# Kernel optimization log

Measured on AMD Instinct MI355X. Metric: run time of the kernel, lower is better.

## Reference

```python
import jax, jax.numpy as jnp
import numpy as np

N_HEAD = 8
WINDOW = 22   # sliding window size from get_mask()
TRAIN = 29    # per-segment length cap from get_mask()


def _build_mask(T):
    # Banded (sliding-window causal) mask on one segment, tiled 3x3 over segments.
    t = T // 3
    m = np.triu(np.ones((TRAIN, TRAIN), dtype=bool), 1)
    for i in range(WINDOW, TRAIN):
        m[i, : i - WINDOW + 1] = True
    m = np.tile(m[:t, :t], (3, 3))  # [T, T], True = masked out
    return jnp.asarray(m)


def setup_inputs() -> dict:
    key = jax.random.key(0)
    ks = jax.random.split(key, 5)
    B, T, C = 512, 87, 512
    s = 0.02
    return {
        "x": jax.random.normal(ks[0], (B, T, C), dtype=jnp.float32),
        "Wq": jax.random.normal(ks[1], (C, C), dtype=jnp.float32) * s,
        "bq": jnp.zeros((C,), dtype=jnp.float32),
        "Wk": jax.random.normal(ks[2], (C, C), dtype=jnp.float32) * s,
        "bk": jnp.zeros((C,), dtype=jnp.float32),
        "Wv": jax.random.normal(ks[3], (C, C), dtype=jnp.float32) * s,
        "bv": jnp.zeros((C,), dtype=jnp.float32),
        "Wp": jax.random.normal(ks[4], (C, C), dtype=jnp.float32) * s,
        "bp": jnp.zeros((C,), dtype=jnp.float32),
    }


def reference(x, Wq, bq, Wk, bk, Wv, bv, Wp, bp):
    B, T, C = x.shape
    H = N_HEAD
    D = C // H
    # nn.Linear: y = x @ W.T + b
    def split_heads(y):
        return y.reshape(B, T, H, D).transpose(0, 2, 1, 3)  # [B,H,T,D]
    q = split_heads(x @ Wq.T + bq)
    k = split_heads(x @ Wk.T + bk)
    v = split_heads(x @ Wv.T + bv)
    att = jnp.einsum("bhqd,bhkd->bhqk", q, k) * (1.0 / jnp.sqrt(jnp.float32(D)))
    mask = _build_mask(T)  # [T,T] True = disallowed
    att = jnp.where(mask[None, None], -jnp.inf, att)
    att = jax.nn.softmax(att, axis=-1)
    # dropout layers are identity in eval mode
    y = jnp.einsum("bhqk,bhkd->bhqd", att, v)
    y = y.transpose(0, 2, 1, 3).reshape(B, T, C)
    return y @ Wp.T + bp
```

## Files before the change

kernel.cpp:

```cpp
#include <hip/hip_runtime.h>
#include <hip/hip_bf16.h>
#include <stdint.h>

#define B_   512
#define T_   87
#define C_   512
#define H_   8
#define D_   64
#define BT_  44544
#define BH_  4096

typedef __attribute__((ext_vector_type(4))) float f32x4;
typedef __attribute__((ext_vector_type(8))) __bf16 bf16x8;
typedef __attribute__((ext_vector_type(4))) unsigned short u16x4;

__device__ __forceinline__ int mod29(int x) {
  return x < 29 ? x : (x < 58 ? x - 29 : x - 58);
}


__global__ void convert_x_kernel(const float* __restrict__ x,
                                 __hip_bfloat16* __restrict__ xb, int n4) {
  int stride = gridDim.x * blockDim.x;
  for (int i = blockIdx.x * blockDim.x + threadIdx.x; i < n4; i += stride) {
    f32x4 v = ((const f32x4*)x)[i];
    u16x4 o;
    o.x = __builtin_bit_cast(unsigned short, __float2bfloat16(v.x));
    o.y = __builtin_bit_cast(unsigned short, __float2bfloat16(v.y));
    o.z = __builtin_bit_cast(unsigned short, __float2bfloat16(v.z));
    o.w = __builtin_bit_cast(unsigned short, __float2bfloat16(v.w));
    ((u16x4*)xb)[i] = o;
  }
}

__global__ void convert_w_kernel(const float* __restrict__ Wq, const float* __restrict__ Wk,
                                 const float* __restrict__ Wv, const float* __restrict__ Wp,
                                 const float* __restrict__ bq, const float* __restrict__ bk,
                                 const float* __restrict__ bv,
                                 __hip_bfloat16* __restrict__ wqkv,
                                 __hip_bfloat16* __restrict__ wp,
                                 float* __restrict__ biasc) {
  const int NW = 262144;
  const int total = 3 * NW + NW + 1536;
  int stride = gridDim.x * blockDim.x;
  for (int i = blockIdx.x * blockDim.x + threadIdx.x; i < total; i += stride) {
    if (i < 3 * NW) {
      float v = (i < NW) ? Wq[i] : (i < 2 * NW ? Wk[i - NW] : Wv[i - 2 * NW]);
      wqkv[i] = __float2bfloat16(v);
    } else if (i < 4 * NW) {
      wp[i - 3 * NW] = __float2bfloat16(Wp[i - 3 * NW]);
    } else {
      int j = i - 4 * NW;
      biasc[j] = (j < 512) ? bq[j] : (j < 1024 ? bk[j - 512] : bv[j - 1024]);
    }
  }
}


template<int EPI>
__global__ __launch_bounds__(256, 4) void gemms_kernel(
    const __hip_bfloat16* __restrict__ A, const __hip_bfloat16* __restrict__ Bt,
    const float* __restrict__ bias, int ntn,
    void* __restrict__ o0, void* __restrict__ o1, void* __restrict__ o2) {
  __shared__ __align__(16) char smem[2][2][8192];

  int tid = threadIdx.x, lane = tid & 63, wave = tid >> 6;
  int r16 = lane & 15, r4 = lane >> 4;

  int nwg = gridDim.x;
  int wg = (blockIdx.x & 7) * (nwg >> 3) + (blockIdx.x >> 3);
  int tileM = (wg / ntn) * 128, tileN = (wg % ntn) * 128;

  int wr = wave >> 1, wc = wave & 1;
  int wbM = wr * 64, wbN = wc * 64;

  const int rl = tid >> 2, c = tid & 3;
  const char* Ag = (const char*)A + (size_t)(tileM + rl) * 1024 + c * 16;
  const char* Bg = (const char*)Bt + (size_t)(tileN + rl) * 1024 + c * 16;
  int lsl[2];
#pragma unroll
  for (int j = 0; j < 2; ++j) {
    int row = rl + 64 * j;
    lsl[j] = row * 64 + ((c ^ ((row >> 1) & 3)) << 4);
  }

  int aoff[4], boff[4];
#pragma unroll
  for (int f = 0; f < 4; ++f) {
    int ra = wbM + f * 16 + r16;
    int rb = wbN + f * 16 + r16;
    aoff[f] = ra * 64 + ((r4 ^ ((ra >> 1) & 3)) << 4);
    boff[f] = rb * 64 + ((r4 ^ ((rb >> 1) & 3)) << 4);
  }

  f32x4 acc[4][4] = {};
  bf16x8 sA[2], sB[2];

#pragma unroll
  for (int j = 0; j < 2; ++j) {
    sA[j] = *(const bf16x8*)(Ag + (size_t)j * 65536);
    sB[j] = *(const bf16x8*)(Bg + (size_t)j * 65536);
  }
#pragma unroll
  for (int j = 0; j < 2; ++j) {
    *(bf16x8*)(&smem[0][0][0] + lsl[j]) = sA[j];
    *(bf16x8*)(&smem[0][1][0] + lsl[j]) = sB[j];
  }
  __syncthreads();

#pragma unroll
  for (int kt = 0; kt < 16; ++kt) {
    const int cur = kt & 1;
    if (kt < 15) {
#pragma unroll
      for (int j = 0; j < 2; ++j) {
        sA[j] = *(const bf16x8*)(Ag + (size_t)j * 65536 + (kt + 1) * 64);
        sB[j] = *(const bf16x8*)(Bg + (size_t)j * 65536 + (kt + 1) * 64);
      }
    }
    {
      const char* Ab = &smem[cur][0][0];
      const char* Bb = &smem[cur][1][0];
      bf16x8 bfr[4];
#pragma unroll
      for (int fn = 0; fn < 4; ++fn) bfr[fn] = *(const bf16x8*)(Bb + boff[fn]);
      __builtin_amdgcn_s_setprio(1);
#pragma unroll
      for (int fm = 0; fm < 4; ++fm) {
        bf16x8 a = *(const bf16x8*)(Ab + aoff[fm]);
#pragma unroll
        for (int fn = 0; fn < 4; ++fn)
          acc[fm][fn] = __builtin_amdgcn_mfma_f32_16x16x32_bf16(a, bfr[fn],
                                                                acc[fm][fn], 0, 0, 0);
      }
      __builtin_amdgcn_s_setprio(0);
    }
    if (kt < 15) {
#pragma unroll
      for (int j = 0; j < 2; ++j) {
        *(bf16x8*)(&smem[cur ^ 1][0][0] + lsl[j]) = sA[j];
        *(bf16x8*)(&smem[cur ^ 1][1][0] + lsl[j]) = sB[j];
      }
    }
    __syncthreads();
  }

  if constexpr (EPI == 0) {
    char* scratch = &smem[0][0][0] + wave * 2304;
    int gn0 = tileN + wbN;
    int sel = gn0 >> 9;
    int hh = (gn0 & 511) >> 6;
    __hip_bfloat16* obase = (sel == 0) ? (__hip_bfloat16*)o0
                          : (sel == 1) ? (__hip_bfloat16*)o1 : (__hip_bfloat16*)o2;
#pragma unroll
    for (int fm = 0; fm < 4; ++fm) {
#pragma unroll
      for (int fn = 0; fn < 4; ++fn) {
        float bv = bias[gn0 + fn * 16 + r16];
#pragma unroll
        for (int rr = 0; rr < 4; ++rr)
          *(__hip_bfloat16*)(scratch + (r4 * 4 + rr) * 144 + (fn * 16 + r16) * 2) =
              __float2bfloat16(acc[fm][fn][rr] + bv);
      }
#pragma unroll
      for (int p = 0; p < 2; ++p) {
        bf16x8 vrow = *(const bf16x8*)(scratch + (p * 8 + (lane >> 3)) * 144 + (lane & 7) * 16);
        int gm = tileM + wbM + fm * 16 + p * 8 + (lane >> 3);
        int bb = gm / 87, tt = gm - bb * 87;
        *(bf16x8*)(obase + ((size_t)(bb * 8 + hh) * 96 + tt) * 64 + (lane & 7) * 8) = vrow;
      }
    }
  } else {
    char* scratch = &smem[0][0][0] + wave * 4352;
#pragma unroll
    for (int fm = 0; fm < 4; ++fm) {
#pragma unroll
      for (int fn = 0; fn < 4; ++fn) {
        float bv = bias[tileN + wbN + fn * 16 + r16];
#pragma unroll
        for (int rr = 0; rr < 4; ++rr)
          *(float*)(scratch + (r4 * 4 + rr) * 272 + (fn * 16 + r16) * 4) =
              acc[fm][fn][rr] + bv;
      }
#pragma unroll
      for (int p = 0; p < 4; ++p) {
        f32x4 vr = *(const f32x4*)(scratch + (p * 4 + (lane >> 4)) * 272 + (lane & 15) * 16);
        int gm = tileM + wbM + fm * 16 + p * 4 + (lane >> 4);
        *(f32x4*)((float*)o0 + (size_t)gm * 512 + tileN + wbN + (lane & 15) * 4) = vr;
      }
    }
  }
}

#define QS_O  0
#define KS_O  13824
#define VT_O  27648
#define PB_O  40960

__global__ __launch_bounds__(256) void attn_kernel(
    const __hip_bfloat16* __restrict__ q_ws, const __hip_bfloat16* __restrict__ k_ws,
    const __hip_bfloat16* __restrict__ v_ws, __hip_bfloat16* __restrict__ y_ws) {
  __shared__ __align__(16) char smem[60928];

  int tid = threadIdx.x, lane = tid & 63, wave = tid >> 6;
  int bh = blockIdx.x, b = bh >> 3, h = bh & 7;
  int r16 = lane & 15, r4 = lane >> 4;

  {
    const bf16x8* gq = (const bf16x8*)(q_ws + (size_t)bh * 6144);
    const bf16x8* gk = (const bf16x8*)(k_ws + (size_t)bh * 6144);
    const bf16x8* gv = (const bf16x8*)(v_ws + (size_t)bh * 6144);
    for (int i = tid; i < 768; i += 256) {
      int row = i >> 3, ch = i & 7;
      *(bf16x8*)(smem + QS_O + row * 144 + ch * 16) = gq[i];
      *(bf16x8*)(smem + KS_O + row * 144 + ch * 16) = gk[i];
      bf16x8 v8 = gv[i];
      int tc = row >> 3, tb = (row & 7) << 1, xr = ch & 3;
#pragma unroll
      for (int e = 0; e < 8; ++e) {
        int d = ch * 8 + e;
        *(__bf16*)(smem + VT_O + d * 208 + ((tc ^ xr) << 4) + tb) = v8[e];
      }
    }
  }
  __syncthreads();

  int ljv[6]; bool cok[6];
#pragma unroll
  for (int j = 0; j < 6; ++j) {
    int col = j * 16 + r16;
    ljv[j] = mod29(col);
    cok[j] = col < 87;
  }

  for (int m = wave; m < 6; m += 4) {
    f32x4 s[6] = {};
#pragma unroll
    for (int kk = 0; kk < 2; ++kk) {
      bf16x8 aq = *(const bf16x8*)(smem + QS_O + (m * 16 + r16) * 144 + kk * 64 + r4 * 16);
#pragma unroll
      for (int j = 0; j < 6; ++j) {
        bf16x8 kb = *(const bf16x8*)(smem + KS_O + (j * 16 + r16) * 144 + kk * 64 + r4 * 16);
        s[j] = __builtin_amdgcn_mfma_f32_16x16x32_bf16(aq, kb, s[j], 0, 0, 0);
      }
    }
#pragma unroll
    for (int rr = 0; rr < 4; ++rr) {
      int row = m * 16 + r4 * 4 + rr;
      bool rok = row < 87;
      int lr = mod29(row);
      float mxv = -1e30f;
#pragma unroll
      for (int j = 0; j < 6; ++j) {
        bool al = rok && cok[j] && (ljv[j] <= lr) && (ljv[j] + 21 >= lr);
        float sv = al ? s[j][rr] * 0.125f : -1e30f;
        s[j][rr] = sv;
        mxv = fmaxf(mxv, sv);
      }
      mxv = fmaxf(mxv, __shfl_xor(mxv, 1));
      mxv = fmaxf(mxv, __shfl_xor(mxv, 2));
      mxv = fmaxf(mxv, __shfl_xor(mxv, 4));
      mxv = fmaxf(mxv, __shfl_xor(mxv, 8));
      float sm = 0.f;
#pragma unroll
      for (int j = 0; j < 6; ++j) {
        float e = __expf(s[j][rr] - mxv);
        s[j][rr] = e;
        sm += e;
      }
      sm += __shfl_xor(sm, 1);
      sm += __shfl_xor(sm, 2);
      sm += __shfl_xor(sm, 4);
      sm += __shfl_xor(sm, 8);
      float inv = rok ? 1.f / sm : 0.f;
#pragma unroll
      for (int j = 0; j < 6; ++j)
        *(__hip_bfloat16*)(smem + PB_O + row * 208 + (j * 16 + r16) * 2) =
            __float2bfloat16(s[j][rr] * inv);
    }
  }
  __syncthreads();

  for (int p = 0; p < 6; ++p) {
    int pair = wave + p * 4;
    int mt = pair >> 2, nt = pair & 3;
    int d = nt * 16 + r16;
    int dx = (d >> 3) & 3;
    f32x4 acc = {0.f, 0.f, 0.f, 0.f};
#pragma unroll
    for (int kk = 0; kk < 3; ++kk) {
      bf16x8 a  = *(const bf16x8*)(smem + PB_O + (mt * 16 + r16) * 208 + kk * 64 + r4 * 16);
      bf16x8 bb = *(const bf16x8*)(smem + VT_O + d * 208 + (((kk * 4 + r4) ^ dx) << 4));
      acc = __builtin_amdgcn_mfma_f32_16x16x32_bf16(a, bb, acc, 0, 0, 0);
    }
    int t0 = mt * 16 + r4 * 4;
#pragma unroll
    for (int r = 0; r < 4; ++r)
      *(__bf16*)(smem + QS_O + (t0 + r) * 136 + d * 2) =
          __builtin_bit_cast(__bf16, __builtin_bit_cast(unsigned short, __float2bfloat16(acc[r])));
  }
  __syncthreads();

  for (int i = tid; i < 768; i += 256) {
    int row = i >> 3, ch = i & 7;
    if (row < 87) {
      bf16x8 vrow = *(const bf16x8*)(smem + QS_O + row * 136 + ch * 16);
      *(bf16x8*)((char*)y_ws + ((size_t)b * 87 + row) * 1024 + h * 128 + ch * 16) = vrow;
    }
  }
}

extern "C" void kernel_launch(void* const* d_in, const int* in_sizes, int n_in,
                              void* d_out, int out_size, void* d_ws, size_t ws_size,
                              hipStream_t stream) {
  const float* x  = (const float*)d_in[0];
  const float* Wq = (const float*)d_in[1];
  const float* bq = (const float*)d_in[2];
  const float* Wk = (const float*)d_in[3];
  const float* bk = (const float*)d_in[4];
  const float* Wv = (const float*)d_in[5];
  const float* bv = (const float*)d_in[6];
  const float* Wp = (const float*)d_in[7];
  const float* bp = (const float*)d_in[8];
  float* out = (float*)d_out;

  char* ws = (char*)d_ws;
  size_t off = 0;
  __hip_bfloat16* xb    = (__hip_bfloat16*)(ws + off); off += (size_t)BT_ * 512 * 2;
  __hip_bfloat16* wqkv  = (__hip_bfloat16*)(ws + off); off += 1536 * 512 * 2;
  __hip_bfloat16* wp    = (__hip_bfloat16*)(ws + off); off += 512 * 512 * 2;
  float*          biasc = (float*)(ws + off);          off += 8192;
  __hip_bfloat16* q_ws  = (__hip_bfloat16*)(ws + off); off += (size_t)BH_ * 6144 * 2;
  __hip_bfloat16* k_ws  = (__hip_bfloat16*)(ws + off); off += (size_t)BH_ * 6144 * 2;
  __hip_bfloat16* v_ws  = (__hip_bfloat16*)(ws + off); off += (size_t)BH_ * 6144 * 2;
  __hip_bfloat16* yb = xb;

  if (ws_size < off) return;

  convert_x_kernel<<<2048, 256, 0, stream>>>(x, xb, BT_ * 512 / 4);
  convert_w_kernel<<<1024, 256, 0, stream>>>(Wq, Wk, Wv, Wp, bq, bk, bv, wqkv, wp, biasc);
  gemms_kernel<0><<<4176, 256, 0, stream>>>(xb, wqkv, biasc, 12, q_ws, k_ws, v_ws);
  attn_kernel<<<BH_, 256, 0, stream>>>(q_ws, k_ws, v_ws, yb);
  gemms_kernel<1><<<1392, 256, 0, stream>>>(yb, wp, bp, 4, out, nullptr, nullptr);
}
```

Before: 239.5 us.

## Load GEMM tiles directly into LDS with global_load_lds and explicit waits

Replaces the register-staged global-to-LDS copy in both GEMMs with the direct global_load_lds path. The XOR swizzle moves from the LDS write address to the global source address, and the loop uses explicit vmcnt waits plus raw s_barrier with scheduling barriers. This is meant to save the VGPRs and ds_write instructions spent on staging, and launch bounds rise from 4 to 5 waves per SIMD to use the freed registers. The risk is correctness of the swizzle-to-source mapping and the barrier ordering around the overwritten buffer.

```diff
diff --git a/kernel.cpp b/kernel.cpp
--- a/kernel.cpp
+++ b/kernel.cpp
@@ -13,6 +13,19 @@
 typedef __attribute__((ext_vector_type(4))) float f32x4;
 typedef __attribute__((ext_vector_type(8))) __bf16 bf16x8;
 typedef __attribute__((ext_vector_type(4))) unsigned short u16x4;
+
+__device__ __forceinline__ void gl_lds16(const void* g, void* l) {
+  __builtin_amdgcn_global_load_lds(
+      (const __attribute__((address_space(1))) unsigned int*)g,
+      (__attribute__((address_space(3))) unsigned int*)l, 16, 0, 0);
+}
+
+template<int N>
+__device__ __forceinline__ void waitv() {
+  asm volatile("s_waitcnt vmcnt(%0)" :: "i"(N) : "memory");
+}
+
+#define PHASE_SEP() __builtin_amdgcn_sched_barrier(0)
 
 __device__ __forceinline__ int mod29(int x) {
   return x < 29 ? x : (x < 58 ? x - 29 : x - 58);
@@ -58,7 +71,7 @@
 
 
 template<int EPI>
-__global__ __launch_bounds__(256, 4) void gemms_kernel(
+__global__ __launch_bounds__(256, 5) void gemmg_kernel(
     const __hip_bfloat16* __restrict__ A, const __hip_bfloat16* __restrict__ Bt,
     const float* __restrict__ bias, int ntn,
     void* __restrict__ o0, void* __restrict__ o1, void* __restrict__ o2) {
@@ -74,14 +87,15 @@
   int wr = wave >> 1, wc = wave & 1;
   int wbM = wr * 64, wbN = wc * 64;
 
-  const int rl = tid >> 2, c = tid & 3;
-  const char* Ag = (const char*)A + (size_t)(tileM + rl) * 1024 + c * 16;
-  const char* Bg = (const char*)Bt + (size_t)(tileN + rl) * 1024 + c * 16;
-  int lsl[2];
+  const int rl0 = tid >> 2, cc = tid & 3;
+  const char* Asrc[2];
+  const char* Bsrc[2];
 #pragma unroll
   for (int j = 0; j < 2; ++j) {
-    int row = rl + 64 * j;
-    lsl[j] = row * 64 + ((c ^ ((row >> 1) & 3)) << 4);
+    int row = rl0 + 64 * j;
+    int colsw = ((cc ^ ((row >> 1) & 3)) << 4);
+    Asrc[j] = (const char*)A + (size_t)(tileM + row) * 1024 + colsw;
+    Bsrc[j] = (const char*)Bt + (size_t)(tileN + row) * 1024 + colsw;
   }
 
   int aoff[4], boff[4];
@@ -94,30 +108,27 @@
   }
 
   f32x4 acc[4][4] = {};
-  bf16x8 sA[2], sB[2];
-
-#pragma unroll
-  for (int j = 0; j < 2; ++j) {
-    sA[j] = *(const bf16x8*)(Ag + (size_t)j * 65536);
-    sB[j] = *(const bf16x8*)(Bg + (size_t)j * 65536);
-  }
-#pragma unroll
-  for (int j = 0; j < 2; ++j) {
-    *(bf16x8*)(&smem[0][0][0] + lsl[j]) = sA[j];
-    *(bf16x8*)(&smem[0][1][0] + lsl[j]) = sB[j];
-  }
-  __syncthreads();
+
+#define STAGE(bufi, kb)                                                         \
+  do {                                                                          \
+    _Pragma("unroll")                                                           \
+    for (int j = 0; j < 2; ++j)                                                 \
+      gl_lds16(Asrc[j] + (kb), &smem[bufi][0][0] + j * 4096 + wave * 1024);     \
+    _Pragma("unroll")                                                           \
+    for (int j = 0; j < 2; ++j)                                                 \
+      gl_lds16(Bsrc[j] + (kb), &smem[bufi][1][0] + j * 4096 + wave * 1024);     \
+  } while (0)
+
+  STAGE(0, 0);
 
 #pragma unroll
   for (int kt = 0; kt < 16; ++kt) {
     const int cur = kt & 1;
-    if (kt < 15) {
-#pragma unroll
-      for (int j = 0; j < 2; ++j) {
-        sA[j] = *(const bf16x8*)(Ag + (size_t)j * 65536 + (kt + 1) * 64);
-        sB[j] = *(const bf16x8*)(Bg + (size_t)j * 65536 + (kt + 1) * 64);
-      }
-    }
+    if (kt < 15) STAGE(cur ^ 1, (kt + 1) * 64);
+    if (kt < 15) waitv<4>(); else waitv<0>();
+    PHASE_SEP();
+    __builtin_amdgcn_s_barrier();
+    PHASE_SEP();
     {
       const char* Ab = &smem[cur][0][0];
       const char* Bb = &smem[cur][1][0];
@@ -135,15 +146,11 @@
       }
       __builtin_amdgcn_s_setprio(0);
     }
-    if (kt < 15) {
-#pragma unroll
-      for (int j = 0; j < 2; ++j) {
-        *(bf16x8*)(&smem[cur ^ 1][0][0] + lsl[j]) = sA[j];
-        *(bf16x8*)(&smem[cur ^ 1][1][0] + lsl[j]) = sB[j];
-      }
-    }
-    __syncthreads();
-  }
+    PHASE_SEP();
+    __builtin_amdgcn_s_barrier();
+    PHASE_SEP();
+  }
+#undef STAGE
 
   if constexpr (EPI == 0) {
     char* scratch = &smem[0][0][0] + wave * 2304;
@@ -339,7 +346,7 @@
 
   convert_x_kernel<<<2048, 256, 0, stream>>>(x, xb, BT_ * 512 / 4);
   convert_w_kernel<<<1024, 256, 0, stream>>>(Wq, Wk, Wv, Wp, bq, bk, bv, wqkv, wp, biasc);
-  gemms_kernel<0><<<4176, 256, 0, stream>>>(xb, wqkv, biasc, 12, q_ws, k_ws, v_ws);
+  gemmg_kernel<0><<<4176, 256, 0, stream>>>(xb, wqkv, biasc, 12, q_ws, k_ws, v_ws);
   attn_kernel<<<BH_, 256, 0, stream>>>(q_ws, k_ws, v_ws, yb);
-  gemms_kernel<1><<<1392, 256, 0, stream>>>(yb, wp, bp, 4, out, nullptr, nullptr);
-}
+  gemmg_kernel<1><<<1392, 256, 0, stream>>>(yb, wp, bp, 4, out, nullptr, nullptr);
+}
```

Measured after the change: 258.8 us. 1.08x slower.

## Use two-wave 128x128 GEMM tiles with 64x128 per-wave subtiles

Applied to the files above, without the earlier changes.

Restructures both projection GEMMs to run 128-thread workgroups, where each of two waves computes a 64x128 output subtile instead of four waves computing 64x64. The aim is more MFMA work per LDS load of B fragments, since each wave reuses its A fragment across eight B fragments. Global-to-LDS loading and the epilogue staging are reworked to match. The cost is doubled accumulator registers per wave and fewer waves per workgroup, which may reduce latency hiding. Scratch in the epilogue grows and must still fit inside the shared buffer.

```diff
diff --git a/kernel.cpp b/kernel.cpp
--- a/kernel.cpp
+++ b/kernel.cpp
@@ -58,7 +58,7 @@
 
 
 template<int EPI>
-__global__ __launch_bounds__(256, 4) void gemms_kernel(
+__global__ __launch_bounds__(128, 2) void gemm2w_kernel(
     const __hip_bfloat16* __restrict__ A, const __hip_bfloat16* __restrict__ Bt,
     const float* __restrict__ bias, int ntn,
     void* __restrict__ o0, void* __restrict__ o1, void* __restrict__ o2) {
@@ -71,38 +71,42 @@
   int wg = (blockIdx.x & 7) * (nwg >> 3) + (blockIdx.x >> 3);
   int tileM = (wg / ntn) * 128, tileN = (wg % ntn) * 128;
 
-  int wr = wave >> 1, wc = wave & 1;
-  int wbM = wr * 64, wbN = wc * 64;
-
-  const int rl = tid >> 2, c = tid & 3;
-  const char* Ag = (const char*)A + (size_t)(tileM + rl) * 1024 + c * 16;
-  const char* Bg = (const char*)Bt + (size_t)(tileN + rl) * 1024 + c * 16;
-  int lsl[2];
-#pragma unroll
-  for (int j = 0; j < 2; ++j) {
-    int row = rl + 64 * j;
-    lsl[j] = row * 64 + ((c ^ ((row >> 1) & 3)) << 4);
-  }
-
-  int aoff[4], boff[4];
+  int wbM = wave * 64;
+
+  const int rl0 = tid >> 2, cc = tid & 3;
+  const char* Ag[4];
+  const char* Bg[4];
+  int lsl[4];
+#pragma unroll
+  for (int j = 0; j < 4; ++j) {
+    int row = rl0 + 32 * j;
+    Ag[j] = (const char*)A + (size_t)(tileM + row) * 1024 + cc * 16;
+    Bg[j] = (const char*)Bt + (size_t)(tileN + row) * 1024 + cc * 16;
+    lsl[j] = row * 64 + ((cc ^ ((row >> 1) & 3)) << 4);
+  }
+
+  int aoff[4], boff[8];
 #pragma unroll
   for (int f = 0; f < 4; ++f) {
     int ra = wbM + f * 16 + r16;
-    int rb = wbN + f * 16 + r16;
     aoff[f] = ra * 64 + ((r4 ^ ((ra >> 1) & 3)) << 4);
+  }
+#pragma unroll
+  for (int f = 0; f < 8; ++f) {
+    int rb = f * 16 + r16;
     boff[f] = rb * 64 + ((r4 ^ ((rb >> 1) & 3)) << 4);
   }
 
-  f32x4 acc[4][4] = {};
-  bf16x8 sA[2], sB[2];
-
-#pragma unroll
-  for (int j = 0; j < 2; ++j) {
-    sA[j] = *(const bf16x8*)(Ag + (size_t)j * 65536);
-    sB[j] = *(const bf16x8*)(Bg + (size_t)j * 65536);
-  }
-#pragma unroll
-  for (int j = 0; j < 2; ++j) {
+  f32x4 acc[4][8] = {};
+  bf16x8 sA[4], sB[4];
+
+#pragma unroll
+  for (int j = 0; j < 4; ++j) {
+    sA[j] = *(const bf16x8*)(Ag[j]);
+    sB[j] = *(const bf16x8*)(Bg[j]);
+  }
+#pragma unroll
+  for (int j = 0; j < 4; ++j) {
     *(bf16x8*)(&smem[0][0][0] + lsl[j]) = sA[j];
     *(bf16x8*)(&smem[0][1][0] + lsl[j]) = sB[j];
   }
@@ -113,23 +117,23 @@
     const int cur = kt & 1;
     if (kt < 15) {
 #pragma unroll
-      for (int j = 0; j < 2; ++j) {
-        sA[j] = *(const bf16x8*)(Ag + (size_t)j * 65536 + (kt + 1) * 64);
-        sB[j] = *(const bf16x8*)(Bg + (size_t)j * 65536 + (kt + 1) * 64);
+      for (int j = 0; j < 4; ++j) {
+        sA[j] = *(const bf16x8*)(Ag[j] + (kt + 1) * 64);
+        sB[j] = *(const bf16x8*)(Bg[j] + (kt + 1) * 64);
       }
     }
     {
       const char* Ab = &smem[cur][0][0];
       const char* Bb = &smem[cur][1][0];
-      bf16x8 bfr[4];
-#pragma unroll
-      for (int fn = 0; fn < 4; ++fn) bfr[fn] = *(const bf16x8*)(Bb + boff[fn]);
+      bf16x8 bfr[8];
+#pragma unroll
+      for (int fn = 0; fn < 8; ++fn) bfr[fn] = *(const bf16x8*)(Bb + boff[fn]);
       __builtin_amdgcn_s_setprio(1);
 #pragma unroll
       for (int fm = 0; fm < 4; ++fm) {
         bf16x8 a = *(const bf16x8*)(Ab + aoff[fm]);
 #pragma unroll
-        for (int fn = 0; fn < 4; ++fn)
+        for (int fn = 0; fn < 8; ++fn)
           acc[fm][fn] = __builtin_amdgcn_mfma_f32_16x16x32_bf16(a, bfr[fn],
                                                                 acc[fm][fn], 0, 0, 0);
       }
@@ -137,7 +141,7 @@
     }
     if (kt < 15) {
 #pragma unroll
-      for (int j = 0; j < 2; ++j) {
+      for (int j = 0; j < 4; ++j) {
         *(bf16x8*)(&smem[cur ^ 1][0][0] + lsl[j]) = sA[j];
         *(bf16x8*)(&smem[cur ^ 1][1][0] + lsl[j]) = sB[j];
       }
@@ -146,47 +150,49 @@
   }
 
   if constexpr (EPI == 0) {
-    char* scratch = &smem[0][0][0] + wave * 2304;
-    int gn0 = tileN + wbN;
-    int sel = gn0 >> 9;
-    int hh = (gn0 & 511) >> 6;
+    char* scratch = &smem[0][0][0] + wave * 4352;
+    int sel = tileN >> 9;
+    int hh0 = (tileN & 511) >> 6;
     __hip_bfloat16* obase = (sel == 0) ? (__hip_bfloat16*)o0
                           : (sel == 1) ? (__hip_bfloat16*)o1 : (__hip_bfloat16*)o2;
 #pragma unroll
     for (int fm = 0; fm < 4; ++fm) {
 #pragma unroll
-      for (int fn = 0; fn < 4; ++fn) {
-        float bv = bias[gn0 + fn * 16 + r16];
+      for (int fn = 0; fn < 8; ++fn) {
+        float bv = bias[tileN + fn * 16 + r16];
 #pragma unroll
         for (int rr = 0; rr < 4; ++rr)
-          *(__hip_bfloat16*)(scratch + (r4 * 4 + rr) * 144 + (fn * 16 + r16) * 2) =
+          *(__hip_bfloat16*)(scratch + (r4 * 4 + rr) * 272 + (fn * 16 + r16) * 2) =
               __float2bfloat16(acc[fm][fn][rr] + bv);
       }
 #pragma unroll
-      for (int p = 0; p < 2; ++p) {
-        bf16x8 vrow = *(const bf16x8*)(scratch + (p * 8 + (lane >> 3)) * 144 + (lane & 7) * 16);
-        int gm = tileM + wbM + fm * 16 + p * 8 + (lane >> 3);
+      for (int p = 0; p < 4; ++p) {
+        bf16x8 vrow = *(const bf16x8*)(scratch + (p * 4 + (lane >> 4)) * 272 + (lane & 15) * 16);
+        int gm = tileM + wbM + fm * 16 + p * 4 + (lane >> 4);
         int bb = gm / 87, tt = gm - bb * 87;
-        *(bf16x8*)(obase + ((size_t)(bb * 8 + hh) * 96 + tt) * 64 + (lane & 7) * 8) = vrow;
+        int col0 = (lane & 15) * 8;
+        int hh = hh0 + (col0 >> 6);
+        int dd = col0 & 63;
+        *(bf16x8*)(obase + ((size_t)(bb * 8 + hh) * 96 + tt) * 64 + dd) = vrow;
       }
     }
   } else {
-    char* scratch = &smem[0][0][0] + wave * 4352;
+    char* scratch = &smem[0][0][0] + wave * 8448;
 #pragma unroll
     for (int fm = 0; fm < 4; ++fm) {
 #pragma unroll
-      for (int fn = 0; fn < 4; ++fn) {
-        float bv = bias[tileN + wbN + fn * 16 + r16];
+      for (int fn = 0; fn < 8; ++fn) {
+        float bv = bias[tileN + fn * 16 + r16];
 #pragma unroll
         for (int rr = 0; rr < 4; ++rr)
-          *(float*)(scratch + (r4 * 4 + rr) * 272 + (fn * 16 + r16) * 4) =
+          *(float*)(scratch + (r4 * 4 + rr) * 528 + (fn * 16 + r16) * 4) =
               acc[fm][fn][rr] + bv;
       }
 #pragma unroll
-      for (int p = 0; p < 4; ++p) {
-        f32x4 vr = *(const f32x4*)(scratch + (p * 4 + (lane >> 4)) * 272 + (lane & 15) * 16);
-        int gm = tileM + wbM + fm * 16 + p * 4 + (lane >> 4);
-        *(f32x4*)((float*)o0 + (size_t)gm * 512 + tileN + wbN + (lane & 15) * 4) = vr;
+      for (int p = 0; p < 8; ++p) {
+        f32x4 vr = *(const f32x4*)(scratch + (p * 2 + (lane >> 5)) * 528 + (lane & 31) * 16);
+        int gm = tileM + wbM + fm * 16 + p * 2 + (lane >> 5);
+        *(f32x4*)((float*)o0 + (size_t)gm * 512 + tileN + (lane & 31) * 4) = vr;
       }
     }
   }
@@ -339,7 +345,7 @@
 
   convert_x_kernel<<<2048, 256, 0, stream>>>(x, xb, BT_ * 512 / 4);
   convert_w_kernel<<<1024, 256, 0, stream>>>(Wq, Wk, Wv, Wp, bq, bk, bv, wqkv, wp, biasc);
-  gemms_kernel<0><<<4176, 256, 0, stream>>>(xb, wqkv, biasc, 12, q_ws, k_ws, v_ws);
+  gemm2w_kernel<0><<<4176, 128, 0, stream>>>(xb, wqkv, biasc, 12, q_ws, k_ws, v_ws);
   attn_kernel<<<BH_, 256, 0, stream>>>(q_ws, k_ws, v_ws, yb);
-  gemms_kernel<1><<<1392, 256, 0, stream>>>(yb, wp, bp, 4, out, nullptr, nullptr);
-}
+  gemm2w_kernel<1><<<1392, 128, 0, stream>>>(yb, wp, bp, 4, out, nullptr, nullptr);
+}
```

After: 246.0 us. +2.7%, slower.
